# Kernel tuning notes

Measured on AMD Instinct MI355X. Metric: run time of the kernel, lower is better.

Reference implementation:

```python
import jax, jax.numpy as jnp
import numpy as np

N, E, W, G = 100000, 625000, 128, 64  # nodes, edges, width, num graphs
EPS = 1e-5


def setup_inputs() -> dict:
    key = jax.random.key(0)
    ks = jax.random.split(key, 8)
    x = jax.random.normal(ks[0], (N, W), jnp.float32)
    edge_index = jax.random.randint(ks[1], (2, E), 0, N, dtype=jnp.int32)
    edge_weight = jax.random.uniform(ks[2], (E,), jnp.float32)
    batch_map = jnp.sort(jax.random.randint(ks[3], (N,), 0, G, dtype=jnp.int32))
    s = 1.0 / np.sqrt(W)
    return {
        "x": x,
        "edge_index": edge_index,
        "edge_weight": edge_weight,
        "batch_map": batch_map,
        "gn_weight": jnp.ones((W,), jnp.float32),
        "gn_bias": jnp.zeros((W,), jnp.float32),
        "gn_mean_scale": jnp.ones((W,), jnp.float32),
        "W_rel1": jax.random.normal(ks[4], (W, W), jnp.float32) * s,
        "b_rel1": jnp.zeros((W,), jnp.float32),
        "W_root1": jax.random.normal(ks[5], (W, W), jnp.float32) * s,
        "W_rel2": jax.random.normal(ks[6], (W, W), jnp.float32) * s,
        "b_rel2": jnp.zeros((W,), jnp.float32),
        "W_root2": jax.random.normal(ks[7], (W, W), jnp.float32) * s,
    }


def _graph_norm(x, batch, weight, bias, mean_scale):
    # per-graph mean / var keyed on batch_map (PyG GraphNorm)
    cnt = jax.ops.segment_sum(jnp.ones((x.shape[0], 1), x.dtype), batch, num_segments=G)
    mean = jax.ops.segment_sum(x, batch, num_segments=G) / cnt
    out = x - mean_scale * mean[batch]
    var = jax.ops.segment_sum(out * out, batch, num_segments=G) / cnt
    std = jnp.sqrt(var + EPS)
    return weight * out / std[batch] + bias


def _graph_conv(x, src, dst, ew, W_rel, b_rel, W_root):
    # out_i = W_rel @ sum_{j->i} e_ji * x_j + b_rel + W_root @ x_i
    msg = x[src] * ew[:, None]                       # [E, W] gather
    agg = jax.ops.segment_sum(msg, dst, num_segments=x.shape[0])  # scatter-add
    return agg @ W_rel.T + b_rel + x @ W_root.T


def reference(x, edge_index, edge_weight, batch_map,
              gn_weight, gn_bias, gn_mean_scale,
              W_rel1, b_rel1, W_root1, W_rel2, b_rel2, W_root2):
    src, dst = edge_index[0], edge_index[1]
    xx = _graph_norm(x, batch_map, gn_weight, gn_bias, gn_mean_scale)
    xx = _graph_conv(xx, src, dst, edge_weight, W_rel1, b_rel1, W_root1)
    xx = jnp.where(xx >= 0, xx, 0.1 * xx)            # LeakyReLU(0.1)
    xx = _graph_conv(xx, src, dst, edge_weight, W_rel2, b_rel2, W_root2)
    return x + xx
```

## Files before the change

kernel.cpp:

```cpp
#include <hip/hip_runtime.h>
#include <hip/hip_bf16.h>

#define WW 128
#define GG 64
#define GN_EPS 1e-5f
#define SCAN_B 1024

typedef __attribute__((ext_vector_type(8))) short short8;
typedef __attribute__((ext_vector_type(4))) float floatx4;

__device__ inline float bf2f(__hip_bfloat16 h) { return __bfloat162float(h); }
__device__ inline float bfbits2f(short v) {
    return __uint_as_float(((unsigned)(unsigned short)v) << 16);
}
__device__ inline short f2bfbits(float f) {
    __hip_bfloat16 h = __float2bfloat16(f);
    return *reinterpret_cast<short*>(&h);
}

__global__ __launch_bounds__(256) void prep1_kernel(
    const int* __restrict__ ei, int E, int* __restrict__ deg, int HB,
    const float* __restrict__ x, const int* __restrict__ batch, int N, int SB,
    float* __restrict__ gsum, float* __restrict__ gsumsq, float* __restrict__ gcnt,
    const float* __restrict__ w0, const float* __restrict__ w1,
    const float* __restrict__ w2, const float* __restrict__ w3,
    __hip_bfloat16* __restrict__ wdst)
{
    int bid = blockIdx.x;
    int tid = threadIdx.x;

    if (bid < HB) {
        int base = bid * 1024 + tid;
        int d0 = (base             < E) ? ei[(size_t)E + base]       : -1;
        int d1 = (base + 256       < E) ? ei[(size_t)E + base + 256] : -1;
        int d2 = (base + 512       < E) ? ei[(size_t)E + base + 512] : -1;
        int d3 = (base + 768       < E) ? ei[(size_t)E + base + 768] : -1;
        if (d0 >= 0) atomicAdd(&deg[d0], 1);
        if (d1 >= 0) atomicAdd(&deg[d1], 1);
        if (d2 >= 0) atomicAdd(&deg[d2], 1);
        if (d3 >= 0) atomicAdd(&deg[d3], 1);
        return;
    }
    if (bid < HB + SB) {
        int sb = bid - HB;
        int half = tid >> 7;
        int w = tid & 127;
        int row0 = sb * 64 + half * 32;
        if (row0 >= N) return;
        int row1 = min(row0 + 32, N);
        float s = 0.f, ss = 0.f;
        int cur = batch[row0];
        int cnt = 0;
        auto flush = [&]() {
            atomicAdd(&gsum[cur * WW + w], s);
            atomicAdd(&gsumsq[cur * WW + w], ss);
            if (w == 0) atomicAdd(&gcnt[cur], (float)cnt);
            s = 0.f; ss = 0.f; cnt = 0;
        };
        int i = row0;
        for (; i + 4 <= row1; i += 4) {
            int g0 = batch[i + 0], g1 = batch[i + 1], g2 = batch[i + 2], g3 = batch[i + 3];
            float v0 = x[(size_t)(i + 0) * WW + w];
            float v1 = x[(size_t)(i + 1) * WW + w];
            float v2 = x[(size_t)(i + 2) * WW + w];
            float v3 = x[(size_t)(i + 3) * WW + w];
            if (g0 != cur) { flush(); cur = g0; }
            s += v0; ss += v0 * v0; ++cnt;
            if (g1 != cur) { flush(); cur = g1; }
            s += v1; ss += v1 * v1; ++cnt;
            if (g2 != cur) { flush(); cur = g2; }
            s += v2; ss += v2 * v2; ++cnt;
            if (g3 != cur) { flush(); cur = g3; }
            s += v3; ss += v3 * v3; ++cnt;
        }
        for (; i < row1; ++i) {
            int g = batch[i];
            float v = x[(size_t)i * WW + w];
            if (g != cur) { flush(); cur = g; }
            s += v; ss += v * v; ++cnt;
        }
        flush();
        return;
    }
    int idx = (bid - HB - SB) * 256 + tid;
    int m = idx >> 14;
    int o = idx & 16383;
    const float* src = (m == 0) ? w0 : (m == 1) ? w1 : (m == 2) ? w2 : w3;
    wdst[idx] = __float2bfloat16(src[o]);
}

__global__ __launch_bounds__(SCAN_B) void scan_blocks(
    const int* __restrict__ deg, int N, int* __restrict__ off, int* __restrict__ bsum)
{
    __shared__ int s[SCAN_B];
    int t = threadIdx.x;
    int i = blockIdx.x * SCAN_B + t;
    int v = (i < N) ? deg[i] : 0;
    s[t] = v; __syncthreads();
    for (int d = 1; d < SCAN_B; d <<= 1) {
        int tmp = (t >= d) ? s[t - d] : 0;
        __syncthreads();
        s[t] += tmp;
        __syncthreads();
    }
    if (i < N) off[i] = s[t] - v;
    if (t == SCAN_B - 1) bsum[blockIdx.x] = s[t];
}

__global__ __launch_bounds__(SCAN_B) void add_offsets2(
    int* __restrict__ off, const int* __restrict__ bsum, int N)
{
    __shared__ int red[SCAN_B];
    int t = threadIdx.x;
    red[t] = (t < blockIdx.x) ? bsum[t] : 0;
    __syncthreads();
    for (int s = SCAN_B / 2; s > 0; s >>= 1) {
        if (t < s) red[t] += red[t + s];
        __syncthreads();
    }
    int i = blockIdx.x * SCAN_B + t;
    if (i < N) off[i] += red[0];
}

__global__ __launch_bounds__(256) void place_fin_kernel(
    const int* __restrict__ ei, const float* __restrict__ ew,
    const int* __restrict__ off, int* __restrict__ cursor,
    int2* __restrict__ ebuf, int E, int PB,
    const float* __restrict__ gsum, const float* __restrict__ gsumsq,
    const float* __restrict__ gcnt,
    const float* __restrict__ wgt, const float* __restrict__ bias,
    const float* __restrict__ ms,
    float* __restrict__ scalev, float* __restrict__ shiftv)
{
    int bid = blockIdx.x;
    int tid = threadIdx.x;

    if (bid < PB) {
        int base = bid * 1024 + tid;
        int dstv[4], srcv[4];
        float wv[4];
        int slot[4];
#pragma unroll
        for (int i = 0; i < 4; ++i) {
            int e = base + i * 256;
            dstv[i] = (e < E) ? ei[(size_t)E + e] : -1;
        }
#pragma unroll
        for (int i = 0; i < 4; ++i) {
            int e = base + i * 256;
            if (e < E) { srcv[i] = ei[e]; wv[i] = ew[e]; }
        }
#pragma unroll
        for (int i = 0; i < 4; ++i)
            if (dstv[i] >= 0) slot[i] = off[dstv[i]] + atomicAdd(&cursor[dstv[i]], 1);
#pragma unroll
        for (int i = 0; i < 4; ++i)
            if (dstv[i] >= 0) {
                unsigned long long v = (unsigned)srcv[i]
                    | ((unsigned long long)__float_as_uint(wv[i]) << 32);
                __builtin_nontemporal_store(v, (unsigned long long*)&ebuf[slot[i]]);
            }
        return;
    }
    int idx = (bid - PB) * 256 + tid;
    if (idx >= GG * WW) return;
    int g = idx >> 7, w = idx & (WW - 1);
    float cnt = gcnt[g];
    float inv = cnt > 0.f ? 1.f / cnt : 0.f;
    float mean = gsum[idx] * inv;
    float msw = ms[w];
    float var = gsumsq[idx] * inv - mean * mean * msw * (2.f - msw);
    var = fmaxf(var, 0.f);
    float sc = wgt[w] * rsqrtf(var + GN_EPS);
    scalev[idx] = sc;
    shiftv[idx] = bias[w] - sc * msw * mean;
}

__global__ __launch_bounds__(256) void normalize_kernel(
    const float* __restrict__ x, const int* __restrict__ batch,
    const float* __restrict__ scalev, const float* __restrict__ shiftv,
    __hip_bfloat16* __restrict__ xn, int N)
{
    size_t tid = (size_t)blockIdx.x * blockDim.x + threadIdx.x;
    if (tid >= (size_t)N * (WW / 8)) return;
    int row = (int)(tid >> 4);
    int c8 = (int)(tid & 15) * 8;
    int g = batch[row];
    const float* xb = x + (size_t)row * WW + c8;
    const float* scb = scalev + (size_t)g * WW + c8;
    const float* shb = shiftv + (size_t)g * WW + c8;
    float4 v0 = *(const float4*)(xb);
    float4 v1 = *(const float4*)(xb + 4);
    float4 sc0 = *(const float4*)(scb);
    float4 sc1 = *(const float4*)(scb + 4);
    float4 sh0 = *(const float4*)(shb);
    float4 sh1 = *(const float4*)(shb + 4);
    union { short s[8]; uint4 u; } pk;
    pk.s[0] = f2bfbits(sc0.x * v0.x + sh0.x);
    pk.s[1] = f2bfbits(sc0.y * v0.y + sh0.y);
    pk.s[2] = f2bfbits(sc0.z * v0.z + sh0.z);
    pk.s[3] = f2bfbits(sc0.w * v0.w + sh0.w);
    pk.s[4] = f2bfbits(sc1.x * v1.x + sh1.x);
    pk.s[5] = f2bfbits(sc1.y * v1.y + sh1.y);
    pk.s[6] = f2bfbits(sc1.z * v1.z + sh1.z);
    pk.s[7] = f2bfbits(sc1.w * v1.w + sh1.w);
    *(uint4*)(xn + (size_t)row * WW + c8) = pk.u;
}

template <bool OUT_BF16>
__global__ __launch_bounds__(256, 4) void fused_kernel(
    const __hip_bfloat16* __restrict__ X,
    const int2* __restrict__ ebuf, const int* __restrict__ off,
    const int* __restrict__ deg,
    const __hip_bfloat16* __restrict__ Wrel, const __hip_bfloat16* __restrict__ Wroot,
    const float* __restrict__ bias, const float* __restrict__ resid,
    void* __restrict__ outv, int N, int leaky)
{
    __shared__ __align__(16) __hip_bfloat16 smem[2 * 32 * 128];
    __shared__ __align__(16) int2 eshare[512];
    int tid = threadIdx.x;
    int wave = tid >> 6, lane = tid & 63;
    int q = lane >> 4, r16 = lane & 15;
    int rb = blockIdx.x * 32;

#pragma unroll
    for (int s = 0; s < 2; ++s) {
        int t = wave * 2 + s;
        int rloc = t * 4 + (lane >> 4);
        int c = (lane & 15) ^ (rloc & 15);
        int grow = rb + rloc; if (grow >= N) grow = N - 1;
        const __hip_bfloat16* g = X + (size_t)grow * WW + c * 8;
        __hip_bfloat16* l = smem + 4096 + t * 512;
        __builtin_amdgcn_global_load_lds(
            (const __attribute__((address_space(1))) void*)g,
            (__attribute__((address_space(3))) void*)l, 16, 0, 0);
    }

    int endn = min(rb + 32, N) - 1;
    int e0 = off[rb];
    int ne = off[endn] + deg[endn] - e0;
    int nstage = min(ne, 512);
    {
        int pairs = (nstage + 1) >> 1;
        if (tid < pairs) {
            const int2* g = ebuf + e0 + 2 * tid;
            int2* l = eshare + 2 * (wave * 64);
            __builtin_amdgcn_global_load_lds(
                (const __attribute__((address_space(1))) void*)g,
                (__attribute__((address_space(3))) void*)l, 16, 0, 0);
        }
    }
    __syncthreads();

    int node = rb + (tid >> 3);
    int nc = node < N ? node : N - 1;
    int start = off[nc];
    int d = (node < N) ? deg[nc] : 0;
    int lb = start - e0;
    int sub = tid & 7;
    float a16[16];
#pragma unroll
    for (int j = 0; j < 16; ++j) a16[j] = 0.f;
    int last = d - 1;
    for (int k = 0; k <= last; k += 4) {
        int j1 = min(k + 1, last);
        int j2 = min(k + 2, last);
        int j3 = min(k + 3, last);
        int2 p0, p1, p2, p3;
        if (lb + j3 < nstage) {
            p0 = eshare[lb + k];
            p1 = eshare[lb + j1];
            p2 = eshare[lb + j2];
            p3 = eshare[lb + j3];
        } else {
            p0 = (lb + k  < nstage) ? eshare[lb + k]  : ebuf[start + k];
            p1 = (lb + j1 < nstage) ? eshare[lb + j1] : ebuf[start + j1];
            p2 = (lb + j2 < nstage) ? eshare[lb + j2] : ebuf[start + j2];
            p3 = (lb + j3 < nstage) ? eshare[lb + j3] : ebuf[start + j3];
        }
        const __hip_bfloat16* r0 = X + (size_t)p0.x * WW + sub * 16;
        const __hip_bfloat16* r1 = X + (size_t)p1.x * WW + sub * 16;
        const __hip_bfloat16* r2 = X + (size_t)p2.x * WW + sub * 16;
        const __hip_bfloat16* r3 = X + (size_t)p3.x * WW + sub * 16;
        short8 a0 = *(const short8*)(r0);
        short8 b0 = *(const short8*)(r0 + 8);
        short8 a1 = *(const short8*)(r1);
        short8 b1 = *(const short8*)(r1 + 8);
        short8 a2 = *(const short8*)(r2);
        short8 b2 = *(const short8*)(r2 + 8);
        short8 a3 = *(const short8*)(r3);
        short8 b3 = *(const short8*)(r3 + 8);
        float w0 = __int_as_float(p0.y);
        float w1 = (k + 1 <= last) ? __int_as_float(p1.y) : 0.f;
        float w2 = (k + 2 <= last) ? __int_as_float(p2.y) : 0.f;
        float w3 = (k + 3 <= last) ? __int_as_float(p3.y) : 0.f;
#pragma unroll
        for (int j = 0; j < 8; ++j) {
            a16[j]     += w0 * bfbits2f(a0[j]) + w1 * bfbits2f(a1[j]);
            a16[8 + j] += w0 * bfbits2f(b0[j]) + w1 * bfbits2f(b1[j]);
            a16[j]     += w2 * bfbits2f(a2[j]) + w3 * bfbits2f(a3[j]);
            a16[8 + j] += w2 * bfbits2f(b2[j]) + w3 * bfbits2f(b3[j]);
        }
    }

    {
        int r = tid >> 3;
        short8 pk0, pk1;
#pragma unroll
        for (int j = 0; j < 8; ++j) {
            pk0[j] = f2bfbits(a16[j]);
            pk1[j] = f2bfbits(a16[8 + j]);
        }
        int s0 = (2 * sub)     ^ (r & 15);
        int s1 = (2 * sub + 1) ^ (r & 15);
        *(short8*)(smem + r * 128 + s0 * 8) = pk0;
        *(short8*)(smem + r * 128 + s1 * 8) = pk1;
    }

    short8 wf[8][2];
#pragma unroll
    for (int kc = 0; kc < 8; ++kc) {
        const __hip_bfloat16* Wsel = (kc < 4) ? Wrel : Wroot;
        int koff = (kc & 3) * 32 + q * 8;
#pragma unroll
        for (int tt = 0; tt < 2; ++tt) {
            int col = wave * 32 + 2 * r16 + tt;
            wf[kc][tt] = *(const short8*)(Wsel + ((size_t)col * WW + koff));
        }
    }
    float bcol[2];
#pragma unroll
    for (int tt = 0; tt < 2; ++tt) bcol[tt] = bias[wave * 32 + 2 * r16 + tt];

    __syncthreads();

    floatx4 acc[2][2];
#pragma unroll
    for (int r = 0; r < 2; ++r)
#pragma unroll
        for (int tt = 0; tt < 2; ++tt) acc[r][tt] = (floatx4){0.f, 0.f, 0.f, 0.f};

#pragma unroll
    for (int kc = 0; kc < 8; ++kc) {
        int m = kc >> 2;
        short8 af[2];
#pragma unroll
        for (int r = 0; r < 2; ++r) {
            int row = r * 16 + r16;
            int slot = ((kc & 3) * 4 + q) ^ r16;
            af[r] = *(const short8*)(&smem[m * 4096 + row * 128 + slot * 8]);
        }
#pragma unroll
        for (int r = 0; r < 2; ++r) {
            acc[r][0] = __builtin_amdgcn_mfma_f32_16x16x32_bf16(af[r], wf[kc][0], acc[r][0], 0, 0, 0);
            acc[r][1] = __builtin_amdgcn_mfma_f32_16x16x32_bf16(af[r], wf[kc][1], acc[r][1], 0, 0, 0);
        }
    }

    int colb = wave * 32 + 2 * r16;
#pragma unroll
    for (int r = 0; r < 2; ++r)
#pragma unroll
        for (int rr = 0; rr < 4; ++rr) {
            int row = rb + r * 16 + q * 4 + rr;
            if (row < N) {
                float v0 = acc[r][0][rr] + bcol[0];
                float v1 = acc[r][1][rr] + bcol[1];
                if (leaky) {
                    v0 = v0 >= 0.f ? v0 : 0.1f * v0;
                    v1 = v1 >= 0.f ? v1 : 0.1f * v1;
                }
                if (OUT_BF16) {
                    __hip_bfloat162 o;
                    o.x = __float2bfloat16(v0);
                    o.y = __float2bfloat16(v1);
                    *(__hip_bfloat162*)((__hip_bfloat16*)outv + (size_t)row * WW + colb) = o;
                } else {
                    float2 rv = *(const float2*)(resid + (size_t)row * WW + colb);
                    float2 o;
                    o.x = v0 + rv.x;
                    o.y = v1 + rv.y;
                    *(float2*)((float*)outv + (size_t)row * WW + colb) = o;
                }
            }
        }
}

extern "C" void kernel_launch(void* const* d_in, const int* in_sizes, int n_in,
                              void* d_out, int out_size, void* d_ws, size_t ws_size,
                              hipStream_t stream) {
    const float* x      = (const float*)d_in[0];
    const int*   ei     = (const int*)d_in[1];
    const float* ew     = (const float*)d_in[2];
    const int*   batch  = (const int*)d_in[3];
    const float* gnw    = (const float*)d_in[4];
    const float* gnb    = (const float*)d_in[5];
    const float* gnm    = (const float*)d_in[6];
    const float* Wrel1  = (const float*)d_in[7];
    const float* brel1  = (const float*)d_in[8];
    const float* Wroot1 = (const float*)d_in[9];
    const float* Wrel2  = (const float*)d_in[10];
    const float* brel2  = (const float*)d_in[11];
    const float* Wroot2 = (const float*)d_in[12];

    int N = in_sizes[0] / WW;
    int E = in_sizes[1] / 2;
    int P = (N + SCAN_B - 1) / SCAN_B;
    int ntiles = (N + 31) / 32;
    int HB = (E + 1023) / 1024;
    int SB = (N + 63) / 64;
    int PB = (E + 1023) / 1024;
    int FB = (GG * WW + 255) / 256;

    __hip_bfloat16* xn = (__hip_bfloat16*)d_ws;
    __hip_bfloat16* y1 = xn + (size_t)N * WW;
    __hip_bfloat16* Wb = y1 + (size_t)N * WW;
    int2* ebuf   = (int2*)(Wb + 4 * WW * WW);
    int*  deg    = (int*)(ebuf + E);
    int*  cursor = deg + N;
    float* gsum   = (float*)(cursor + N);
    float* gsumsq = gsum + GG * WW;
    float* gcnt   = gsumsq + GG * WW;
    float* scalev = gcnt + GG;
    float* shiftv = scalev + GG * WW;
    int*  off    = (int*)(shiftv + GG * WW);
    int*  bsum   = off + N;

    hipMemsetAsync(deg, 0, ((size_t)2 * N + 2 * GG * WW + GG) * sizeof(int), stream);

    prep1_kernel<<<HB + SB + 256, 256, 0, stream>>>(
        ei, E, deg, HB,
        x, batch, N, SB, gsum, gsumsq, gcnt,
        Wrel1, Wroot1, Wrel2, Wroot2, Wb);

    scan_blocks<<<P, SCAN_B, 0, stream>>>(deg, N, off, bsum);
    add_offsets2<<<P, SCAN_B, 0, stream>>>(off, bsum, N);

    place_fin_kernel<<<PB + FB, 256, 0, stream>>>(
        ei, ew, off, cursor, ebuf, E, PB,
        gsum, gsumsq, gcnt, gnw, gnb, gnm, scalev, shiftv);

    normalize_kernel<<<(int)(((size_t)N * (WW / 8) + 255) / 256), 256, 0, stream>>>(
        x, batch, scalev, shiftv, xn, N);

    fused_kernel<true><<<ntiles, 256, 0, stream>>>(
        xn, ebuf, off, deg, Wb, Wb + WW * WW, brel1, nullptr, y1, N, 1);

    fused_kernel<false><<<ntiles, 256, 0, stream>>>(
        y1, ebuf, off, deg, Wb + 2 * WW * WW, Wb + 3 * WW * WW, brel2, x, d_out, N, 0);
}
```

Before: 313.7 us.

## Edge-parallel LDS atomic aggregation in fused conv; merge prep kernels to cut launches

The fused conv kernel stops giving one 8-thread group per destination node. It now walks the tile's edges edge-parallel, finds each edge's destination node by binary search over a shared offset table, and accumulates weighted neighbour rows into a float LDS buffer with atomic adds. Tiles with more than 512 edges fall back to a per-node register loop. Separately, the GN finalize step moves into the scan kernel and normalization merges with edge placement, removing one launch. The goal is to balance load across uneven node degrees. The cost is many LDS float atomics, 16KB more shared memory per block (lower occupancy), and an extra pass to read agg back.

New measurement: 1.099 ms. 3.5x slower.

```diff
diff --git a/kernel.cpp b/kernel.cpp
--- a/kernel.cpp
+++ b/kernel.cpp
@@ -9,13 +9,22 @@
 typedef __attribute__((ext_vector_type(8))) short short8;
 typedef __attribute__((ext_vector_type(4))) float floatx4;
 
-__device__ inline float bf2f(__hip_bfloat16 h) { return __bfloat162float(h); }
 __device__ inline float bfbits2f(short v) {
     return __uint_as_float(((unsigned)(unsigned short)v) << 16);
 }
 __device__ inline short f2bfbits(float f) {
     __hip_bfloat16 h = __float2bfloat16(f);
     return *reinterpret_cast<short*>(&h);
+}
+
+__device__ inline int node_of(const int* soff, int e) {
+    int lo = 0;
+#pragma unroll
+    for (int s = 16; s > 0; s >>= 1) {
+        int cand = lo + s;
+        if (soff[cand] <= e) lo = cand;
+    }
+    return lo;
 }
 
 __global__ __launch_bounds__(256) void prep1_kernel(
@@ -31,10 +40,10 @@
 
     if (bid < HB) {
         int base = bid * 1024 + tid;
-        int d0 = (base             < E) ? ei[(size_t)E + base]       : -1;
-        int d1 = (base + 256       < E) ? ei[(size_t)E + base + 256] : -1;
-        int d2 = (base + 512       < E) ? ei[(size_t)E + base + 512] : -1;
-        int d3 = (base + 768       < E) ? ei[(size_t)E + base + 768] : -1;
+        int d0 = (base       < E) ? ei[(size_t)E + base]       : -1;
+        int d1 = (base + 256 < E) ? ei[(size_t)E + base + 256] : -1;
+        int d2 = (base + 512 < E) ? ei[(size_t)E + base + 512] : -1;
+        int d3 = (base + 768 < E) ? ei[(size_t)E + base + 768] : -1;
         if (d0 >= 0) atomicAdd(&deg[d0], 1);
         if (d1 >= 0) atomicAdd(&deg[d1], 1);
         if (d2 >= 0) atomicAdd(&deg[d2], 1);
@@ -89,43 +98,8 @@
     wdst[idx] = __float2bfloat16(src[o]);
 }
 
-__global__ __launch_bounds__(SCAN_B) void scan_blocks(
-    const int* __restrict__ deg, int N, int* __restrict__ off, int* __restrict__ bsum)
-{
-    __shared__ int s[SCAN_B];
-    int t = threadIdx.x;
-    int i = blockIdx.x * SCAN_B + t;
-    int v = (i < N) ? deg[i] : 0;
-    s[t] = v; __syncthreads();
-    for (int d = 1; d < SCAN_B; d <<= 1) {
-        int tmp = (t >= d) ? s[t - d] : 0;
-        __syncthreads();
-        s[t] += tmp;
-        __syncthreads();
-    }
-    if (i < N) off[i] = s[t] - v;
-    if (t == SCAN_B - 1) bsum[blockIdx.x] = s[t];
-}
-
-__global__ __launch_bounds__(SCAN_B) void add_offsets2(
-    int* __restrict__ off, const int* __restrict__ bsum, int N)
-{
-    __shared__ int red[SCAN_B];
-    int t = threadIdx.x;
-    red[t] = (t < blockIdx.x) ? bsum[t] : 0;
-    __syncthreads();
-    for (int s = SCAN_B / 2; s > 0; s >>= 1) {
-        if (t < s) red[t] += red[t + s];
-        __syncthreads();
-    }
-    int i = blockIdx.x * SCAN_B + t;
-    if (i < N) off[i] += red[0];
-}
-
-__global__ __launch_bounds__(256) void place_fin_kernel(
-    const int* __restrict__ ei, const float* __restrict__ ew,
-    const int* __restrict__ off, int* __restrict__ cursor,
-    int2* __restrict__ ebuf, int E, int PB,
+__global__ __launch_bounds__(SCAN_B) void scan2_kernel(
+    const int* __restrict__ deg, int N, int* __restrict__ off, int* __restrict__ bsum, int P,
     const float* __restrict__ gsum, const float* __restrict__ gsumsq,
     const float* __restrict__ gcnt,
     const float* __restrict__ wgt, const float* __restrict__ bias,
@@ -133,36 +107,23 @@
     float* __restrict__ scalev, float* __restrict__ shiftv)
 {
     int bid = blockIdx.x;
-    int tid = threadIdx.x;
-
-    if (bid < PB) {
-        int base = bid * 1024 + tid;
-        int dstv[4], srcv[4];
-        float wv[4];
-        int slot[4];
-#pragma unroll
-        for (int i = 0; i < 4; ++i) {
-            int e = base + i * 256;
-            dstv[i] = (e < E) ? ei[(size_t)E + e] : -1;
-        }
-#pragma unroll
-        for (int i = 0; i < 4; ++i) {
-            int e = base + i * 256;
-            if (e < E) { srcv[i] = ei[e]; wv[i] = ew[e]; }
-        }
-#pragma unroll
-        for (int i = 0; i < 4; ++i)
-            if (dstv[i] >= 0) slot[i] = off[dstv[i]] + atomicAdd(&cursor[dstv[i]], 1);
-#pragma unroll
-        for (int i = 0; i < 4; ++i)
-            if (dstv[i] >= 0) {
-                unsigned long long v = (unsigned)srcv[i]
-                    | ((unsigned long long)__float_as_uint(wv[i]) << 32);
-                __builtin_nontemporal_store(v, (unsigned long long*)&ebuf[slot[i]]);
-            }
+    int t = threadIdx.x;
+    if (bid < P) {
+        __shared__ int s[SCAN_B];
+        int i = bid * SCAN_B + t;
+        int v = (i < N) ? deg[i] : 0;
+        s[t] = v; __syncthreads();
+        for (int d = 1; d < SCAN_B; d <<= 1) {
+            int tmp = (t >= d) ? s[t - d] : 0;
+            __syncthreads();
+            s[t] += tmp;
+            __syncthreads();
+        }
+        if (i < N) off[i] = s[t] - v;
+        if (t == SCAN_B - 1) bsum[bid] = s[t];
         return;
     }
-    int idx = (bid - PB) * 256 + tid;
+    int idx = (bid - P) * SCAN_B + t;
     if (idx >= GG * WW) return;
     int g = idx >> 7, w = idx & (WW - 1);
     float cnt = gcnt[g];
@@ -176,15 +137,63 @@
     shiftv[idx] = bias[w] - sc * msw * mean;
 }
 
-__global__ __launch_bounds__(256) void normalize_kernel(
+__global__ __launch_bounds__(SCAN_B) void add_offsets2(
+    int* __restrict__ off, const int* __restrict__ bsum, int N)
+{
+    __shared__ int red[SCAN_B];
+    int t = threadIdx.x;
+    red[t] = (t < blockIdx.x) ? bsum[t] : 0;
+    __syncthreads();
+    for (int s = SCAN_B / 2; s > 0; s >>= 1) {
+        if (t < s) red[t] += red[t + s];
+        __syncthreads();
+    }
+    int i = blockIdx.x * SCAN_B + t;
+    if (i < N) off[i] += red[0];
+}
+
+__global__ __launch_bounds__(256) void place_norm_kernel(
+    const int* __restrict__ ei, const float* __restrict__ ew,
+    const int* __restrict__ off, int* __restrict__ cursor,
+    int2* __restrict__ ebuf, int E, int PB,
     const float* __restrict__ x, const int* __restrict__ batch,
     const float* __restrict__ scalev, const float* __restrict__ shiftv,
     __hip_bfloat16* __restrict__ xn, int N)
 {
-    size_t tid = (size_t)blockIdx.x * blockDim.x + threadIdx.x;
-    if (tid >= (size_t)N * (WW / 8)) return;
-    int row = (int)(tid >> 4);
-    int c8 = (int)(tid & 15) * 8;
+    int bid = blockIdx.x;
+    int tid = threadIdx.x;
+
+    if (bid < PB) {
+        int base = bid * 1024 + tid;
+        int dstv[4], srcv[4];
+        float wv[4];
+        int slot[4];
+#pragma unroll
+        for (int i = 0; i < 4; ++i) {
+            int e = base + i * 256;
+            dstv[i] = (e < E) ? ei[(size_t)E + e] : -1;
+        }
+#pragma unroll
+        for (int i = 0; i < 4; ++i) {
+            int e = base + i * 256;
+            if (e < E) { srcv[i] = ei[e]; wv[i] = ew[e]; }
+        }
+#pragma unroll
+        for (int i = 0; i < 4; ++i)
+            if (dstv[i] >= 0) slot[i] = off[dstv[i]] + atomicAdd(&cursor[dstv[i]], 1);
+#pragma unroll
+        for (int i = 0; i < 4; ++i)
+            if (dstv[i] >= 0) {
+                unsigned long long v = (unsigned)srcv[i]
+                    | ((unsigned long long)__float_as_uint(wv[i]) << 32);
+                __builtin_nontemporal_store(v, (unsigned long long*)&ebuf[slot[i]]);
+            }
+        return;
+    }
+    size_t nt = (size_t)(bid - PB) * 256 + tid;
+    if (nt >= (size_t)N * (WW / 8)) return;
+    int row = (int)(nt >> 4);
+    int c8 = (int)(nt & 15) * 8;
     int g = batch[row];
     const float* xb = x + (size_t)row * WW + c8;
     const float* scb = scalev + (size_t)g * WW + c8;
@@ -217,7 +226,9 @@
     void* __restrict__ outv, int N, int leaky)
 {
     __shared__ __align__(16) __hip_bfloat16 smem[2 * 32 * 128];
+    __shared__ __align__(16) float agg[32 * 128];
     __shared__ __align__(16) int2 eshare[512];
+    __shared__ int soff[33];
     int tid = threadIdx.x;
     int wave = tid >> 6, lane = tid & 63;
     int q = lane >> 4, r16 = lane & 15;
@@ -250,88 +261,130 @@
                 (__attribute__((address_space(3))) void*)l, 16, 0, 0);
         }
     }
+    if (tid <= 32) {
+        int n = rb + tid;
+        soff[tid] = (n < N) ? (off[n] - e0) : ne;
+    }
+#pragma unroll
+    for (int j = 0; j < 16; ++j) agg[tid + 256 * j] = 0.f;
+
     __syncthreads();
 
-    int node = rb + (tid >> 3);
-    int nc = node < N ? node : N - 1;
-    int start = off[nc];
-    int d = (node < N) ? deg[nc] : 0;
-    int lb = start - e0;
+    int g8 = tid >> 3;
     int sub = tid & 7;
-    float a16[16];
-#pragma unroll
-    for (int j = 0; j < 16; ++j) a16[j] = 0.f;
-    int last = d - 1;
-    for (int k = 0; k <= last; k += 4) {
-        int j1 = min(k + 1, last);
-        int j2 = min(k + 2, last);
-        int j3 = min(k + 3, last);
-        int2 p0, p1, p2, p3;
-        if (lb + j3 < nstage) {
-            p0 = eshare[lb + k];
-            p1 = eshare[lb + j1];
-            p2 = eshare[lb + j2];
-            p3 = eshare[lb + j3];
-        } else {
-            p0 = (lb + k  < nstage) ? eshare[lb + k]  : ebuf[start + k];
-            p1 = (lb + j1 < nstage) ? eshare[lb + j1] : ebuf[start + j1];
-            p2 = (lb + j2 < nstage) ? eshare[lb + j2] : ebuf[start + j2];
-            p3 = (lb + j3 < nstage) ? eshare[lb + j3] : ebuf[start + j3];
-        }
-        const __hip_bfloat16* r0 = X + (size_t)p0.x * WW + sub * 16;
-        const __hip_bfloat16* r1 = X + (size_t)p1.x * WW + sub * 16;
-        const __hip_bfloat16* r2 = X + (size_t)p2.x * WW + sub * 16;
-        const __hip_bfloat16* r3 = X + (size_t)p3.x * WW + sub * 16;
-        short8 a0 = *(const short8*)(r0);
-        short8 b0 = *(const short8*)(r0 + 8);
-        short8 a1 = *(const short8*)(r1);
-        short8 b1 = *(const short8*)(r1 + 8);
-        short8 a2 = *(const short8*)(r2);
-        short8 b2 = *(const short8*)(r2 + 8);
-        short8 a3 = *(const short8*)(r3);
-        short8 b3 = *(const short8*)(r3 + 8);
-        float w0 = __int_as_float(p0.y);
-        float w1 = (k + 1 <= last) ? __int_as_float(p1.y) : 0.f;
-        float w2 = (k + 2 <= last) ? __int_as_float(p2.y) : 0.f;
-        float w3 = (k + 3 <= last) ? __int_as_float(p3.y) : 0.f;
-#pragma unroll
-        for (int j = 0; j < 8; ++j) {
-            a16[j]     += w0 * bfbits2f(a0[j]) + w1 * bfbits2f(a1[j]);
-            a16[8 + j] += w0 * bfbits2f(b0[j]) + w1 * bfbits2f(b1[j]);
-            a16[j]     += w2 * bfbits2f(a2[j]) + w3 * bfbits2f(a3[j]);
-            a16[8 + j] += w2 * bfbits2f(b2[j]) + w3 * bfbits2f(b3[j]);
-        }
-    }
+    int gw = g8 & 7;
+
+    if (ne <= 512) {
+        for (int e = g8; e < ne; e += 128) {
+            int c1 = e + 32, c2 = e + 64, c3 = e + 96;
+            bool v1 = c1 < ne, v2 = c2 < ne, v3 = c3 < ne;
+            int f1 = v1 ? c1 : e, f2 = v2 ? c2 : e, f3 = v3 ? c3 : e;
+            int2 p0 = eshare[e];
+            int2 p1 = eshare[f1];
+            int2 p2 = eshare[f2];
+            int2 p3 = eshare[f3];
+            const __hip_bfloat16* r0 = X + (size_t)p0.x * WW + sub * 8;
+            const __hip_bfloat16* r1 = X + (size_t)p1.x * WW + sub * 8;
+            const __hip_bfloat16* r2 = X + (size_t)p2.x * WW + sub * 8;
+            const __hip_bfloat16* r3 = X + (size_t)p3.x * WW + sub * 8;
+            short8 a0 = *(const short8*)(r0);
+            short8 b0 = *(const short8*)(r0 + 64);
+            short8 a1 = *(const short8*)(r1);
+            short8 b1 = *(const short8*)(r1 + 64);
+            short8 a2 = *(const short8*)(r2);
+            short8 b2 = *(const short8*)(r2 + 64);
+            short8 a3 = *(const short8*)(r3);
+            short8 b3 = *(const short8*)(r3 + 64);
+            float w0 = __int_as_float(p0.y);
+            float w1 = __int_as_float(p1.y);
+            float w2 = __int_as_float(p2.y);
+            float w3 = __int_as_float(p3.y);
+            int n0 = node_of(soff, e);
+            int n1 = node_of(soff, f1);
+            int n2 = node_of(soff, f2);
+            int n3 = node_of(soff, f3);
+            float* d0 = &agg[n0 * 128 + sub * 8];
+            float* d1 = &agg[n1 * 128 + sub * 8];
+            float* d2 = &agg[n2 * 128 + sub * 8];
+            float* d3 = &agg[n3 * 128 + sub * 8];
+#pragma unroll
+            for (int jj = 0; jj < 8; ++jj) {
+                int j = (jj + gw) & 7;
+                atomicAdd(d0 + j,      w0 * bfbits2f(a0[j]));
+                atomicAdd(d0 + 64 + j, w0 * bfbits2f(b0[j]));
+                if (v1) { atomicAdd(d1 + j,      w1 * bfbits2f(a1[j]));
+                          atomicAdd(d1 + 64 + j, w1 * bfbits2f(b1[j])); }
+                if (v2) { atomicAdd(d2 + j,      w2 * bfbits2f(a2[j]));
+                          atomicAdd(d2 + 64 + j, w2 * bfbits2f(b2[j])); }
+                if (v3) { atomicAdd(d3 + j,      w3 * bfbits2f(a3[j]));
+                          atomicAdd(d3 + 64 + j, w3 * bfbits2f(b3[j])); }
+            }
+        }
+    } else {
+        int node = rb + g8;
+        float a16[16];
+#pragma unroll
+        for (int j = 0; j < 16; ++j) a16[j] = 0.f;
+        if (node < N) {
+            int start = off[node];
+            int d = deg[node];
+            for (int k = 0; k < d; k += 2) {
+                int k1 = (k + 1 < d) ? k + 1 : k;
+                int2 p0 = ebuf[start + k];
+                int2 p1 = ebuf[start + k1];
+                const __hip_bfloat16* r0 = X + (size_t)p0.x * WW + sub * 8;
+                const __hip_bfloat16* r1 = X + (size_t)p1.x * WW + sub * 8;
+                short8 a0 = *(const short8*)(r0);
+                short8 b0 = *(const short8*)(r0 + 64);
+                short8 a1 = *(const short8*)(r1);
+                short8 b1 = *(const short8*)(r1 + 64);
+                float w0 = __int_as_float(p0.y);
+                float w1 = (k + 1 < d) ? __int_as_float(p1.y) : 0.f;
+#pragma unroll
+                for (int j = 0; j < 8; ++j) {
+                    a16[j]     += w0 * bfbits2f(a0[j]) + w1 * bfbits2f(a1[j]);
+                    a16[8 + j] += w0 * bfbits2f(b0[j]) + w1 * bfbits2f(b1[j]);
+                }
+            }
+            float* dstf = &agg[g8 * 128 + sub * 8];
+#pragma unroll
+            for (int j = 0; j < 8; ++j) {
+                dstf[j]      = a16[j];
+                dstf[64 + j] = a16[8 + j];
+            }
+        }
+    }
+
+    short8 wf[8][2];
+#pragma unroll
+    for (int kc = 0; kc < 8; ++kc) {
+        const __hip_bfloat16* Wsel = (kc < 4) ? Wrel : Wroot;
+        int koff = (kc & 3) * 32 + q * 8;
+#pragma unroll
+        for (int tt = 0; tt < 2; ++tt) {
+            int col = wave * 32 + 2 * r16 + tt;
+            wf[kc][tt] = *(const short8*)(Wsel + ((size_t)col * WW + koff));
+        }
+    }
+    float bcol[2];
+#pragma unroll
+    for (int tt = 0; tt < 2; ++tt) bcol[tt] = bias[wave * 32 + 2 * r16 + tt];
+
+    __syncthreads();
 
     {
         int r = tid >> 3;
         short8 pk0, pk1;
 #pragma unroll
         for (int j = 0; j < 8; ++j) {
-            pk0[j] = f2bfbits(a16[j]);
-            pk1[j] = f2bfbits(a16[8 + j]);
+            pk0[j] = f2bfbits(agg[r * 128 + sub * 16 + j]);
+            pk1[j] = f2bfbits(agg[r * 128 + sub * 16 + 8 + j]);
         }
         int s0 = (2 * sub)     ^ (r & 15);
         int s1 = (2 * sub + 1) ^ (r & 15);
         *(short8*)(smem + r * 128 + s0 * 8) = pk0;
         *(short8*)(smem + r * 128 + s1 * 8) = pk1;
     }
-
-    short8 wf[8][2];
-#pragma unroll
-    for (int kc = 0; kc < 8; ++kc) {
-        const __hip_bfloat16* Wsel = (kc < 4) ? Wrel : Wroot;
-        int koff = (kc & 3) * 32 + q * 8;
-#pragma unroll
-        for (int tt = 0; tt < 2; ++tt) {
-            int col = wave * 32 + 2 * r16 + tt;
-            wf[kc][tt] = *(const short8*)(Wsel + ((size_t)col * WW + koff));
-        }
-    }
-    float bcol[2];
-#pragma unroll
-    for (int tt = 0; tt < 2; ++tt) bcol[tt] = bias[wave * 32 + 2 * r16 + tt];
-
     __syncthreads();
 
     floatx4 acc[2][2];
@@ -410,7 +463,8 @@
     int HB = (E + 1023) / 1024;
     int SB = (N + 63) / 64;
     int PB = (E + 1023) / 1024;
-    int FB = (GG * WW + 255) / 256;
+    int FB2 = (GG * WW + SCAN_B - 1) / SCAN_B;
+    int NB = (int)(((size_t)N * (WW / 8) + 255) / 256);
 
     __hip_bfloat16* xn = (__hip_bfloat16*)d_ws;
     __hip_bfloat16* y1 = xn + (size_t)N * WW;
@@ -433,14 +487,14 @@
         x, batch, N, SB, gsum, gsumsq, gcnt,
         Wrel1, Wroot1, Wrel2, Wroot2, Wb);
 
-    scan_blocks<<<P, SCAN_B, 0, stream>>>(deg, N, off, bsum);
+    scan2_kernel<<<P + FB2, SCAN_B, 0, stream>>>(
+        deg, N, off, bsum, P,
+        gsum, gsumsq, gcnt, gnw, gnb, gnm, scalev, shiftv);
+
     add_offsets2<<<P, SCAN_B, 0, stream>>>(off, bsum, N);
 
-    place_fin_kernel<<<PB + FB, 256, 0, stream>>>(
+    place_norm_kernel<<<PB + NB, 256, 0, stream>>>(
         ei, ew, off, cursor, ebuf, E, PB,
-        gsum, gsumsq, gcnt, gnw, gnb, gnm, scalev, shiftv);
-
-    normalize_kernel<<<(int)(((size_t)N * (WW / 8) + 255) / 256), 256, 0, stream>>>(
         x, batch, scalev, shiftv, xn, N);
 
     fused_kernel<true><<<ntiles, 256, 0, stream>>>(
```
